# Kernel optimization log

Measured on AMD Instinct MI355X. Metric: run time of the kernel, lower is better.

Reference implementation:

```python
import jax, jax.numpy as jnp
import numpy as np


def _cheb_conv(x, row, col, norm, W, b, num_nodes):
    # PyG ChebConv with sym normalization and lambda_max=2:
    # L_hat = -D^{-1/2} A D^{-1/2} (off-diagonal), diagonal exactly 0.
    # Tx_0 = x; Tx_1 = L_hat x; Tx_k = 2 L_hat Tx_{k-1} - Tx_{k-2}
    K = W.shape[0]
    Tx0 = x
    out = Tx0 @ W[0]
    Tx1 = jax.ops.segment_sum(norm[:, None] * Tx0[col], row, num_segments=num_nodes)
    out = out + Tx1 @ W[1]
    for k in range(2, K):
        Tx2 = 2.0 * jax.ops.segment_sum(norm[:, None] * Tx1[col], row, num_segments=num_nodes) - Tx0
        out = out + Tx2 @ W[k]
        Tx0, Tx1 = Tx1, Tx2
    return out + b


def setup_inputs() -> dict:
    key = jax.random.key(0)
    ks = jax.random.split(key, 8)
    N, E, D, H, C, K = 100000, 1600000, 128, 64, 5, 3
    x = jax.random.normal(ks[0], (N, D), dtype=jnp.float32)
    edge_index = jax.random.randint(ks[1], (2, E), 0, N, dtype=jnp.int64)
    edge_weight = jax.random.uniform(ks[2], (E,), dtype=jnp.float32)
    s1 = 1.0 / np.sqrt(D)
    s3 = 1.0 / np.sqrt(H)
    W1 = jax.random.normal(ks[3], (K, D, H), dtype=jnp.float32) * s1
    W3 = jax.random.normal(ks[4], (K, H, H), dtype=jnp.float32) * s3
    W4 = jax.random.normal(ks[5], (K, H, C), dtype=jnp.float32) * s3
    return {
        "x": x, "edge_index": edge_index, "edge_weight": edge_weight,
        "W1": W1, "b1": jnp.zeros((H,), jnp.float32),
        "W3": W3, "b3": jnp.zeros((H,), jnp.float32),
        "W4": W4, "b4": jnp.zeros((C,), jnp.float32),
    }


def reference(x, edge_index, edge_weight, W1, b1, W3, b3, W4, b4):
    N = x.shape[0]
    row, col = edge_index[0], edge_index[1]
    # symmetric normalization of the scaled Laplacian (lambda_max = 2)
    deg = jax.ops.segment_sum(edge_weight, row, num_segments=N)
    dinv = jnp.where(deg > 0, jax.lax.rsqrt(jnp.where(deg > 0, deg, 1.0)), 0.0)
    norm = -dinv[row] * edge_weight * dinv[col]
    # dropout is a no-op in eval mode (training=False)
    h = jax.nn.relu(_cheb_conv(x, row, col, norm, W1, b1, N))
    h = jax.nn.relu(_cheb_conv(h, row, col, norm, W3, b3, N))
    h = _cheb_conv(h, row, col, norm, W4, b4, N)
    return jax.nn.log_softmax(h, axis=1)
```

## Files before the change

kernel.cpp:

```cpp
#include <hip/hip_runtime.h>
#include <cstdint>
#include <cstddef>

typedef unsigned short u16;
typedef __attribute__((ext_vector_type(8))) short bf16x8;
typedef __attribute__((ext_vector_type(4))) float f32x4;

#define PB 1024
#define MAXSB 256
#define SB 512
#define CAP 12288

__device__ __forceinline__ float bflo(unsigned u) { return __uint_as_float(u << 16); }
__device__ __forceinline__ float bfhi(unsigned u) { return __uint_as_float(u & 0xFFFF0000u); }
__device__ __forceinline__ u16 f2bf(float f) {
    unsigned u = __float_as_uint(f);
    u += 0x7FFFu + ((u >> 16) & 1u);
    return (u16)(u >> 16);
}
__device__ __forceinline__ unsigned pack2(float a, float b) {
    return (unsigned)f2bf(a) | ((unsigned)f2bf(b) << 16);
}


__global__ __launch_bounds__(256) void binA(const int* __restrict__ row, int* __restrict__ P,
                                            int E, int NB, int EB) {
    __shared__ int hist[MAXSB];
    int b = blockIdx.x;
    hist[threadIdx.x] = 0;
    __syncthreads();
    int e0 = b * EB, e1 = min(E, e0 + EB);
    for (int e = e0 + threadIdx.x; e < e1; e += 256)
        atomicAdd(&hist[row[e] >> 9], 1);
    __syncthreads();
    if (threadIdx.x < NB) P[(size_t)threadIdx.x * PB + b] = hist[threadIdx.x];
}

__global__ __launch_bounds__(256) void binB1(int* __restrict__ P, int* __restrict__ bintot) {
    __shared__ int sh[256];
    int* p = P + (size_t)blockIdx.x * PB;
    int tid = threadIdx.x;
    int base = tid * 4;
    int v[4];
#pragma unroll
    for (int j = 0; j < 4; ++j) v[j] = p[base + j];
    int s = v[0] + v[1] + v[2] + v[3];
    sh[tid] = s;
    __syncthreads();
    for (int off = 1; off < 256; off <<= 1) {
        int t = (tid >= off) ? sh[tid - off] : 0;
        __syncthreads();
        sh[tid] += t;
        __syncthreads();
    }
    int run = sh[tid] - s;
#pragma unroll
    for (int j = 0; j < 4; ++j) { p[base + j] = run; run += v[j]; }
    if (tid == 255) bintot[blockIdx.x] = sh[255];
}

__device__ __forceinline__ void bs_scan(int* bs, const int* bintot, int NB, int tid) {
    bs[tid] = (tid < NB) ? bintot[tid] : 0;
    __syncthreads();
    for (int off = 1; off < 256; off <<= 1) {
        int t = (tid >= off) ? bs[tid - off] : 0;
        __syncthreads();
        bs[tid] += t;
        __syncthreads();
    }
}

__global__ __launch_bounds__(256) void binC(const int* __restrict__ row, const int* __restrict__ col,
                                            const float* __restrict__ w, const int* __restrict__ P,
                                            const int* __restrict__ bintot, int2* __restrict__ rec,
                                            int E, int NB, int EB) {
    __shared__ int bs[MAXSB];
    __shared__ int cur[MAXSB];
    int b = blockIdx.x;
    int tid = threadIdx.x;
    bs_scan(bs, bintot, NB, tid);
    if (tid < NB) cur[tid] = (tid ? bs[tid - 1] : 0) + P[(size_t)tid * PB + b];
    __syncthreads();
    int e0 = b * EB, e1 = min(E, e0 + EB);
    for (int e = e0 + tid; e < e1; e += 256) {
        int r = row[e];
        int bin = r >> 9;
        int slot = atomicAdd(&cur[bin], 1);
        rec[slot] = make_int2(col[e] | ((r & 511) << 17), __float_as_int(w[e]));
    }
}

__global__ __launch_bounds__(256) void binD1(const int2* __restrict__ rec,
                                             const int* __restrict__ bintot,
                                             int* __restrict__ rowp, float* __restrict__ dinv,
                                             int N, int NB) {
    __shared__ int bs[MAXSB];
    __shared__ int cnt[SB];
    __shared__ float deg[SB];
    __shared__ int wsum[4];
    int bin = blockIdx.x;
    int tid = threadIdx.x;
    bs_scan(bs, bintot, NB, tid);
    int e0 = bin ? bs[bin - 1] : 0;
    int e1 = bs[bin];
    cnt[tid] = 0; cnt[tid + 256] = 0;
    deg[tid] = 0.f; deg[tid + 256] = 0.f;
    __syncthreads();
    for (int e = e0 + tid; e < e1; e += 256) {
        int2 v = rec[e];
        int rl = (v.x >> 17) & 511;
        atomicAdd(&cnt[rl], 1);
        atomicAdd(&deg[rl], __int_as_float(v.y));
    }
    __syncthreads();
    int a = cnt[2 * tid], b = cnt[2 * tid + 1];
    int p = a + b;
    int lane = tid & 63, wv = tid >> 6;
    int incl = p;
    for (int off = 1; off < 64; off <<= 1) {
        int t = __shfl_up(incl, off);
        if (lane >= off) incl += t;
    }
    if (lane == 63) wsum[wv] = incl;
    __syncthreads();
    if (tid == 0) {
        int s = 0;
#pragma unroll
        for (int i = 0; i < 4; ++i) { int t = wsum[i]; wsum[i] = s; s += t; }
    }
    __syncthreads();
    int excl = incl - p + wsum[wv];
    int base = bin * SB;
    int rows = min(SB, N - base);
    if (2 * tid < rows) {
        rowp[base + 2 * tid] = e0 + excl;
        float d = deg[2 * tid];
        dinv[base + 2 * tid] = d > 0.f ? rsqrtf(d) : 0.f;
    }
    if (2 * tid + 1 < rows) {
        rowp[base + 2 * tid + 1] = e0 + excl + a;
        float d = deg[2 * tid + 1];
        dinv[base + 2 * tid + 1] = d > 0.f ? rsqrtf(d) : 0.f;
    }
    if (bin == NB - 1 && tid == 0) rowp[N] = e1;
}

__global__ __launch_bounds__(256) void binD2(const int2* __restrict__ rec,
                                             const int* __restrict__ bintot,
                                             const int* __restrict__ rowp,
                                             const float* __restrict__ dinv,
                                             int2* __restrict__ meta, int N, int NB) {
    __shared__ int bs[MAXSB];
    __shared__ int cur[SB];
    __shared__ int perm[CAP];
    int bin = blockIdx.x;
    int tid = threadIdx.x;
    bs_scan(bs, bintot, NB, tid);
    int e0 = bin ? bs[bin - 1] : 0;
    int e1 = bs[bin];
    int base = bin * SB;
    int rows = min(SB, N - base);
    for (int i = tid; i < rows; i += 256) cur[i] = rowp[base + i];
    __syncthreads();
    for (int e = e0 + tid; e < e1; e += 256) {
        int2 v = rec[e];
        int rl = (v.x >> 17) & 511;
        int slot = atomicAdd(&cur[rl], 1);
        int so = slot - e0;
        if (so < CAP) {
            perm[so] = e - e0;
        } else {
            int c = v.x & 0x1FFFF;
            float ev = -dinv[base + rl] * __int_as_float(v.y) * dinv[c];
            meta[slot] = make_int2(c, __float_as_int(ev));
        }
    }
    __syncthreads();
    int lim = min(e1 - e0, CAP);
    for (int s = tid; s < lim; s += 256) {
        int2 v = rec[e0 + perm[s]];
        int rl = (v.x >> 17) & 511;
        int c = v.x & 0x1FFFF;
        float ev = -dinv[base + rl] * __int_as_float(v.y) * dinv[c];
        meta[e0 + s] = make_int2(c, __float_as_int(ev));
    }
}

__global__ void prep(const float* __restrict__ x, unsigned* __restrict__ xb, int n2,
                     const float* __restrict__ W1, const float* __restrict__ W3,
                     const float* __restrict__ W4, u16* __restrict__ Wpu,
                     u16* __restrict__ Wp3, u16* __restrict__ Wpp) {
    int gi = blockIdx.x * blockDim.x + threadIdx.x;
    if (gi < 3072) {
        int idx = gi;
        int lane = idx & 63;
        int nt = (idx >> 6) % 12;
        int kt = idx / 768;
        int krow = kt * 32 + (lane >> 4) * 8;
        int c = nt * 16 + (lane & 15);
        u16 tmp[8];
#pragma unroll
        for (int j = 0; j < 8; ++j) {
            int k = krow + j;
            float v;
            if (c < 64)       v = W1[(size_t)k * 64 + c] - W1[2 * 8192 + (size_t)k * 64 + c];
            else if (c < 128) v = W1[8192 + (size_t)k * 64 + (c - 64)];
            else              v = W1[2 * 8192 + (size_t)k * 64 + (c - 128)];
            tmp[j] = f2bf(v);
        }
        *reinterpret_cast<uint4*>(Wpu + (size_t)idx * 8) = *reinterpret_cast<const uint4*>(tmp);
    } else if (gi < 3072 + 1536) {
        int idx = gi - 3072;
        int lane = idx & 63;
        int nt = (idx >> 6) & 3;
        int kt = idx >> 8;
        int krow = kt * 32 + (lane >> 4) * 8;
        int c = nt * 16 + (lane & 15);
        u16 tmp[8];
#pragma unroll
        for (int j = 0; j < 8; ++j) tmp[j] = f2bf(W3[(size_t)(krow + j) * 64 + c]);
        *reinterpret_cast<uint4*>(Wp3 + (size_t)idx * 8) = *reinterpret_cast<const uint4*>(tmp);
    } else if (gi < 3072 + 1536 + 256) {
        int idx = gi - (3072 + 1536);
        int lane = idx & 63;
        int nt = (idx >> 6) & 1;
        int kt = idx >> 7;
        int krow = kt * 32 + (lane >> 4) * 8;
        int c = nt * 16 + (lane & 15);
        u16 tmp[8];
#pragma unroll
        for (int j = 0; j < 8; ++j) {
            int k = krow + j;
            float v = 0.f;
            if (c < 5)                  v = W4[(size_t)k * 5 + c] - W4[640 + (size_t)k * 5 + c];
            else if (c >= 8 && c < 13)  v = W4[320 + (size_t)k * 5 + (c - 8)];
            else if (c >= 16 && c < 21) v = W4[640 + (size_t)k * 5 + (c - 16)];
            tmp[j] = f2bf(v);
        }
        *reinterpret_cast<uint4*>(Wpp + (size_t)idx * 8) = *reinterpret_cast<const uint4*>(tmp);
    } else {
        int i = gi - 4864;
        if (i < n2) {
            float2 v = reinterpret_cast<const float2*>(x)[i];
            xb[i] = pack2(v.x, v.y);
        }
    }
}

template <int MODE>
__global__ __launch_bounds__(256) void spmm64(const int* __restrict__ rp,
                                              const int2* __restrict__ meta,
                                              const u16* __restrict__ x,
                                              const u16* __restrict__ z,
                                              const float* __restrict__ bias,
                                              u16* __restrict__ y, int n) {
    int r = blockIdx.x * 16 + (threadIdx.x >> 4);
    if (r >= n) return;
    int sub = (threadIdx.x >> 3) & 1;
    int f = (threadIdx.x & 7) * 8;
    int e0 = rp[r], e1 = rp[r + 1];
    float acc[8] = {0.f, 0.f, 0.f, 0.f, 0.f, 0.f, 0.f, 0.f};
    auto fma8 = [&](uint4 xv, float w) {
        acc[0] += w * bflo(xv.x); acc[1] += w * bfhi(xv.x);
        acc[2] += w * bflo(xv.y); acc[3] += w * bfhi(xv.y);
        acc[4] += w * bflo(xv.z); acc[5] += w * bfhi(xv.z);
        acc[6] += w * bflo(xv.w); acc[7] += w * bfhi(xv.w);
    };
    int e = e0 + sub;
    for (; e + 6 < e1; e += 8) {
        int2 m0 = meta[e], m1 = meta[e + 2], m2 = meta[e + 4], m3 = meta[e + 6];
        uint4 v0 = *reinterpret_cast<const uint4*>(x + (size_t)m0.x * 64 + f);
        uint4 v1 = *reinterpret_cast<const uint4*>(x + (size_t)m1.x * 64 + f);
        uint4 v2 = *reinterpret_cast<const uint4*>(x + (size_t)m2.x * 64 + f);
        uint4 v3 = *reinterpret_cast<const uint4*>(x + (size_t)m3.x * 64 + f);
        fma8(v0, __int_as_float(m0.y));
        fma8(v1, __int_as_float(m1.y));
        fma8(v2, __int_as_float(m2.y));
        fma8(v3, __int_as_float(m3.y));
    }
    for (; e < e1; e += 2) {
        int2 m = meta[e];
        uint4 xv = *reinterpret_cast<const uint4*>(x + (size_t)m.x * 64 + f);
        fma8(xv, __int_as_float(m.y));
    }
#pragma unroll
    for (int j = 0; j < 8; ++j) acc[j] += __shfl_xor(acc[j], 8);
    if (sub) return;
    if (MODE == 1 || MODE == 2) {
        uint4 zv = *reinterpret_cast<const uint4*>(z + (size_t)r * 64 + f);
        float zz[8] = {bflo(zv.x), bfhi(zv.x), bflo(zv.y), bfhi(zv.y),
                       bflo(zv.z), bfhi(zv.z), bflo(zv.w), bfhi(zv.w)};
#pragma unroll
        for (int j = 0; j < 8; ++j)
            acc[j] = (MODE == 1) ? 2.f * acc[j] + zz[j] : 2.f * acc[j] - zz[j];
    } else if (MODE == 3) {
        uint4 zv = *reinterpret_cast<const uint4*>(z + (size_t)r * 64 + f);
        float zz[8] = {bflo(zv.x), bfhi(zv.x), bflo(zv.y), bfhi(zv.y),
                       bflo(zv.z), bfhi(zv.z), bflo(zv.w), bfhi(zv.w)};
        float4 bl = *reinterpret_cast<const float4*>(bias + f);
        float4 bh = *reinterpret_cast<const float4*>(bias + f + 4);
        float bb[8] = {bl.x, bl.y, bl.z, bl.w, bh.x, bh.y, bh.z, bh.w};
#pragma unroll
        for (int j = 0; j < 8; ++j) acc[j] = fmaxf(acc[j] + zz[j] + bb[j], 0.f);
    }
    uint4 o;
    o.x = pack2(acc[0], acc[1]);
    o.y = pack2(acc[2], acc[3]);
    o.z = pack2(acc[4], acc[5]);
    o.w = pack2(acc[6], acc[7]);
    *reinterpret_cast<uint4*>(y + (size_t)r * 64 + f) = o;
}

__device__ __forceinline__ void spmm8_acc(const int* rp, const int2* meta, const u16* x,
                                          int r, int t, float* acc) {
    int e0 = rp[r], e1 = rp[r + 1];
    auto fma8 = [&](uint4 xv, float w) {
        acc[0] += w * bflo(xv.x); acc[1] += w * bfhi(xv.x);
        acc[2] += w * bflo(xv.y); acc[3] += w * bfhi(xv.y);
        acc[4] += w * bflo(xv.z); acc[5] += w * bfhi(xv.z);
        acc[6] += w * bflo(xv.w); acc[7] += w * bfhi(xv.w);
    };
    int e = e0 + t;
    for (; e + 4 < e1; e += 8) {
        int2 m0 = meta[e], m1 = meta[e + 4];
        uint4 v0 = *reinterpret_cast<const uint4*>(x + (size_t)m0.x * 8);
        uint4 v1 = *reinterpret_cast<const uint4*>(x + (size_t)m1.x * 8);
        fma8(v0, __int_as_float(m0.y));
        fma8(v1, __int_as_float(m1.y));
    }
    for (; e < e1; e += 4) {
        int2 m = meta[e];
        uint4 xv = *reinterpret_cast<const uint4*>(x + (size_t)m.x * 8);
        fma8(xv, __int_as_float(m.y));
    }
#pragma unroll
    for (int j = 0; j < 8; ++j) acc[j] += __shfl_xor(acc[j], 1);
#pragma unroll
    for (int j = 0; j < 8; ++j) acc[j] += __shfl_xor(acc[j], 2);
}

__global__ __launch_bounds__(256) void spmm8_p2(const int* __restrict__ rp,
                                                const int2* __restrict__ meta,
                                                const u16* __restrict__ x,
                                                const u16* __restrict__ z,
                                                u16* __restrict__ y, int n) {
    int r = blockIdx.x * 64 + (threadIdx.x >> 2);
    if (r >= n) return;
    int t = threadIdx.x & 3;
    float acc[8] = {0.f, 0.f, 0.f, 0.f, 0.f, 0.f, 0.f, 0.f};
    spmm8_acc(rp, meta, x, r, t, acc);
    if (t == 0) {
        uint4 zv = *reinterpret_cast<const uint4*>(z + (size_t)r * 8);
        float zz[8] = {bflo(zv.x), bfhi(zv.x), bflo(zv.y), bfhi(zv.y),
                       bflo(zv.z), bfhi(zv.z), bflo(zv.w), bfhi(zv.w)};
        uint4 o;
        o.x = pack2(2.f * acc[0] + zz[0], 2.f * acc[1] + zz[1]);
        o.y = pack2(2.f * acc[2] + zz[2], 2.f * acc[3] + zz[3]);
        o.z = pack2(2.f * acc[4] + zz[4], 2.f * acc[5] + zz[5]);
        o.w = pack2(2.f * acc[6] + zz[6], 2.f * acc[7] + zz[7]);
        *reinterpret_cast<uint4*>(y + (size_t)r * 8) = o;
    }
}

__global__ __launch_bounds__(256) void spmm8_lsm(const int* __restrict__ rp,
                                                 const int2* __restrict__ meta,
                                                 const u16* __restrict__ x,
                                                 const u16* __restrict__ z,
                                                 const float* __restrict__ bias,
                                                 float* __restrict__ out, int n) {
    int r = blockIdx.x * 64 + (threadIdx.x >> 2);
    if (r >= n) return;
    int t = threadIdx.x & 3;
    float acc[8] = {0.f, 0.f, 0.f, 0.f, 0.f, 0.f, 0.f, 0.f};
    spmm8_acc(rp, meta, x, r, t, acc);
    if (t == 0) {
        uint4 zv = *reinterpret_cast<const uint4*>(z + (size_t)r * 8);
        float zz[8] = {bflo(zv.x), bfhi(zv.x), bflo(zv.y), bfhi(zv.y),
                       bflo(zv.z), bfhi(zv.z), bflo(zv.w), bfhi(zv.w)};
        float val[5];
#pragma unroll
        for (int j = 0; j < 5; ++j) val[j] = acc[j] + zz[j] + bias[j];
        float mx = val[0];
#pragma unroll
        for (int j = 1; j < 5; ++j) mx = fmaxf(mx, val[j]);
        float s = 0.f;
#pragma unroll
        for (int j = 0; j < 5; ++j) s += expf(val[j] - mx);
        float l = logf(s);
#pragma unroll
        for (int j = 0; j < 5; ++j) out[(size_t)r * 5 + j] = val[j] - mx - l;
    }
}


__global__ __launch_bounds__(256) void gemm_u(const u16* __restrict__ A,
                                              const u16* __restrict__ Wp,
                                              u16* __restrict__ u0, u16* __restrict__ u1,
                                              u16* __restrict__ u2, int n) {
    int wave = threadIdx.x >> 6;
    int lane = threadIdx.x & 63;
    int r0 = blockIdx.x * 64 + wave * 16;
    int row = r0 + (lane & 15);
    int rowc = row < n ? row : n - 1;
    int kofs = (lane >> 4) * 8;
    f32x4 acc[12] = {};
    for (int kt = 0; kt < 4; ++kt) {
        bf16x8 a = *reinterpret_cast<const bf16x8*>(A + (size_t)rowc * 128 + kt * 32 + kofs);
        const u16* wb = Wp + (size_t)kt * 12 * 512 + (size_t)lane * 8;
#pragma unroll
        for (int nt = 0; nt < 12; ++nt) {
            bf16x8 b = *reinterpret_cast<const bf16x8*>(wb + nt * 512);
            acc[nt] = __builtin_amdgcn_mfma_f32_16x16x32_bf16(a, b, acc[nt], 0, 0, 0);
        }
    }
    int col = lane & 15;
    u16* U[3] = {u0, u1, u2};
#pragma unroll
    for (int nt = 0; nt < 12; ++nt) {
        u16* dst = U[nt >> 2];
        int cc = (nt & 3) * 16 + col;
#pragma unroll
        for (int i = 0; i < 4; ++i) {
            int rr = r0 + (lane >> 4) * 4 + i;
            if (rr < n) dst[(size_t)rr * 64 + cc] = f2bf(acc[nt][i]);
        }
    }
}

__global__ __launch_bounds__(256) void gemm3_mfma(const u16* __restrict__ A0,
                                                  const u16* __restrict__ A1,
                                                  const u16* __restrict__ A2,
                                                  const u16* __restrict__ Wp,
                                                  const float* __restrict__ bias,
                                                  u16* __restrict__ out, int n) {
    int wave = threadIdx.x >> 6;
    int lane = threadIdx.x & 63;
    int r0 = blockIdx.x * 64 + wave * 16;
    int row = r0 + (lane & 15);
    int rowc = row < n ? row : n - 1;
    int kofs = (lane >> 4) * 8;
    const u16* Ap[3] = {A0, A1, A2};
    f32x4 acc[4] = {};
    for (int kt = 0; kt < 6; ++kt) {
        const u16* Asrc = Ap[kt >> 1];
        int c0 = (kt & 1) * 32;
        bf16x8 a = *reinterpret_cast<const bf16x8*>(Asrc + (size_t)rowc * 64 + c0 + kofs);
        const u16* wb = Wp + (size_t)kt * 4 * 512 + (size_t)lane * 8;
#pragma unroll
        for (int nt = 0; nt < 4; ++nt) {
            bf16x8 b = *reinterpret_cast<const bf16x8*>(wb + nt * 512);
            acc[nt] = __builtin_amdgcn_mfma_f32_16x16x32_bf16(a, b, acc[nt], 0, 0, 0);
        }
    }
    int col = lane & 15;
#pragma unroll
    for (int nt = 0; nt < 4; ++nt) {
        float bb = bias[nt * 16 + col];
#pragma unroll
        for (int i = 0; i < 4; ++i) {
            int rr = r0 + (lane >> 4) * 4 + i;
            if (rr < n) {
                float v = fmaxf(acc[nt][i] + bb, 0.f);
                out[(size_t)rr * 64 + nt * 16 + col] = f2bf(v);
            }
        }
    }
}

__global__ __launch_bounds__(256) void gemm_proj(const u16* __restrict__ A,
                                                 const u16* __restrict__ Wp,
                                                 u16* __restrict__ p0, u16* __restrict__ p1,
                                                 u16* __restrict__ p2, int n) {
    int wave = threadIdx.x >> 6;
    int lane = threadIdx.x & 63;
    int r0 = blockIdx.x * 64 + wave * 16;
    int row = r0 + (lane & 15);
    int rowc = row < n ? row : n - 1;
    int kofs = (lane >> 4) * 8;
    f32x4 acc[2] = {};
    for (int kt = 0; kt < 2; ++kt) {
        bf16x8 a = *reinterpret_cast<const bf16x8*>(A + (size_t)rowc * 64 + kt * 32 + kofs);
        const u16* wb = Wp + (size_t)kt * 2 * 512 + (size_t)lane * 8;
#pragma unroll
        for (int nt = 0; nt < 2; ++nt) {
            bf16x8 b = *reinterpret_cast<const bf16x8*>(wb + nt * 512);
            acc[nt] = __builtin_amdgcn_mfma_f32_16x16x32_bf16(a, b, acc[nt], 0, 0, 0);
        }
    }
    int col = lane & 15;
    u16* P[3] = {p0, p1, p2};
#pragma unroll
    for (int nt = 0; nt < 2; ++nt) {
        int c = nt * 16 + col;
        if (c < 24) {
            u16* dst = P[c >> 3];
            int j = c & 7;
#pragma unroll
            for (int i = 0; i < 4; ++i) {
                int rr = r0 + (lane >> 4) * 4 + i;
                if (rr < n) dst[(size_t)rr * 8 + j] = f2bf(acc[nt][i]);
            }
        }
    }
}


static inline size_t alignup(size_t v) { return (v + 255) & ~(size_t)255; }

extern "C" void kernel_launch(void* const* d_in, const int* in_sizes, int n_in,
                              void* d_out, int out_size, void* d_ws, size_t ws_size,
                              hipStream_t stream) {
    const float* x  = (const float*)d_in[0];
    const int*   ei = (const int*)d_in[1];
    const float* ew = (const float*)d_in[2];
    const float* W1 = (const float*)d_in[3];
    const float* b1 = (const float*)d_in[4];
    const float* W3 = (const float*)d_in[5];
    const float* b3 = (const float*)d_in[6];
    const float* W4 = (const float*)d_in[7];
    const float* b4 = (const float*)d_in[8];
    float* out = (float*)d_out;

    const int D = 128, H = 64;
    const int N = in_sizes[0] / D;
    const int E = in_sizes[2];
    const int* row = ei;
    const int* col = ei + E;

    char* ws = (char*)d_ws;
    size_t off = 0;
    auto alloc = [&](size_t bytes) { size_t o = off; off += alignup(bytes); return o; };

    float* dinv   = (float*)(ws + alloc((size_t)N * 4));
    int*   rowp   = (int*)  (ws + alloc((size_t)(N + 1) * 4));
    int*   bintot = (int*)  (ws + alloc(MAXSB * 4));
    int*   P      = (int*)  (ws + alloc((size_t)MAXSB * PB * 4));
    int2*  meta   = (int2*) (ws + alloc((size_t)E * 8));
    int2*  rec    = (int2*) (ws + alloc((size_t)E * 8));
    u16*   xb     = (u16*)  (ws + alloc((size_t)N * D * 2));
    u16*   A      = (u16*)  (ws + alloc((size_t)N * H * 2));
    u16*   B      = (u16*)  (ws + alloc((size_t)N * H * 2));
    u16*   C      = (u16*)  (ws + alloc((size_t)N * H * 2));
    u16*   Dd     = (u16*)  (ws + alloc((size_t)N * H * 2));
    u16*   P0     = (u16*)  (ws + alloc((size_t)N * 8 * 2));
    u16*   P1     = (u16*)  (ws + alloc((size_t)N * 8 * 2));
    u16*   P2     = (u16*)  (ws + alloc((size_t)N * 8 * 2));
    u16*   P3     = (u16*)  (ws + alloc((size_t)N * 8 * 2));
    u16*   Wpu    = (u16*)  (ws + alloc((size_t)4 * 12 * 512 * 2));
    u16*   Wp3    = (u16*)  (ws + alloc((size_t)6 * 4 * 512 * 2));
    u16*   Wpp    = (u16*)  (ws + alloc((size_t)2 * 2 * 512 * 2));

    const int NB = (N + SB - 1) / SB;
    const int EB = (E + PB - 1) / PB;

    dim3 blk(256);

    binA<<<PB, blk, 0, stream>>>(row, P, E, NB, EB);
    binB1<<<NB, blk, 0, stream>>>(P, bintot);
    binC<<<PB, blk, 0, stream>>>(row, col, ew, P, bintot, rec, E, NB, EB);
    binD1<<<NB, blk, 0, stream>>>(rec, bintot, rowp, dinv, N, NB);
    binD2<<<NB, blk, 0, stream>>>(rec, bintot, rowp, dinv, meta, N, NB);

    int n2 = N * D / 2;
    prep<<<(n2 + 4864 + 255) / 256, blk, 0, stream>>>(x, (unsigned*)xb, n2, W1, W3, W4,
                                                      Wpu, Wp3, Wpp);

    int g64 = (N + 15) / 16;
    int gG  = (N + 63) / 64;
    int g8  = (N + 63) / 64;

    gemm_u<<<gG, blk, 0, stream>>>(xb, Wpu, A, B, C, N);
    spmm64<1><<<g64, blk, 0, stream>>>(rowp, meta, C, B, nullptr, Dd, N);
    spmm64<3><<<g64, blk, 0, stream>>>(rowp, meta, Dd, A, b1, B, N);

    spmm64<0><<<g64, blk, 0, stream>>>(rowp, meta, B, nullptr, nullptr, C, N);
    spmm64<2><<<g64, blk, 0, stream>>>(rowp, meta, C, B, nullptr, A, N);
    gemm3_mfma<<<gG, blk, 0, stream>>>(B, C, A, Wp3, b3, Dd, N);

    gemm_proj<<<gG, blk, 0, stream>>>(Dd, Wpp, P0, P1, P2, N);
    spmm8_p2<<<g8, blk, 0, stream>>>(rowp, meta, P2, P1, P3, N);
    spmm8_lsm<<<g8, blk, 0, stream>>>(rowp, meta, P3, P0, b4, out, N);
}
```

Before: 285.2 us.

## Fuse x bf16 conversion into gemm_u and projection GEMM into layer-2 GEMM

Drops the separate pass that converts x from fp32 to bf16; gemm_u now reads fp32 x directly and converts in registers. Fuses gemm_proj into gemm3 by staging the relu'd hidden tile in shared memory, so the intermediate 64-wide hidden matrix is never written to or read back from global memory. This removes the xb buffer traffic and one kernel launch, in exchange for a __syncthreads, LDS use and doubled fp32 read bandwidth in gemm_u.

```diff
diff --git a/kernel.cpp b/kernel.cpp
--- a/kernel.cpp
+++ b/kernel.cpp
@@ -186,8 +186,7 @@
     }
 }
 
-__global__ void prep(const float* __restrict__ x, unsigned* __restrict__ xb, int n2,
-                     const float* __restrict__ W1, const float* __restrict__ W3,
+__global__ void prep(const float* __restrict__ W1, const float* __restrict__ W3,
                      const float* __restrict__ W4, u16* __restrict__ Wpu,
                      u16* __restrict__ Wp3, u16* __restrict__ Wpp) {
     int gi = blockIdx.x * blockDim.x + threadIdx.x;
@@ -238,12 +237,6 @@
             tmp[j] = f2bf(v);
         }
         *reinterpret_cast<uint4*>(Wpp + (size_t)idx * 8) = *reinterpret_cast<const uint4*>(tmp);
-    } else {
-        int i = gi - 4864;
-        if (i < n2) {
-            float2 v = reinterpret_cast<const float2*>(x)[i];
-            xb[i] = pack2(v.x, v.y);
-        }
     }
 }
 
@@ -393,7 +386,7 @@
 }
 
 
-__global__ __launch_bounds__(256) void gemm_u(const u16* __restrict__ A,
+__global__ __launch_bounds__(256) void gemm_u(const float* __restrict__ X,
                                               const u16* __restrict__ Wp,
                                               u16* __restrict__ u0, u16* __restrict__ u1,
                                               u16* __restrict__ u2, int n) {
@@ -405,7 +398,12 @@
     int kofs = (lane >> 4) * 8;
     f32x4 acc[12] = {};
     for (int kt = 0; kt < 4; ++kt) {
-        bf16x8 a = *reinterpret_cast<const bf16x8*>(A + (size_t)rowc * 128 + kt * 32 + kofs);
+        const float* xs = X + (size_t)rowc * 128 + kt * 32 + kofs;
+        float4 xa = *reinterpret_cast<const float4*>(xs);
+        float4 xb4 = *reinterpret_cast<const float4*>(xs + 4);
+        u16 tmp[8] = {f2bf(xa.x), f2bf(xa.y), f2bf(xa.z), f2bf(xa.w),
+                      f2bf(xb4.x), f2bf(xb4.y), f2bf(xb4.z), f2bf(xb4.w)};
+        bf16x8 a = *reinterpret_cast<const bf16x8*>(tmp);
         const u16* wb = Wp + (size_t)kt * 12 * 512 + (size_t)lane * 8;
 #pragma unroll
         for (int nt = 0; nt < 12; ++nt) {
@@ -427,12 +425,15 @@
     }
 }
 
-__global__ __launch_bounds__(256) void gemm3_mfma(const u16* __restrict__ A0,
-                                                  const u16* __restrict__ A1,
-                                                  const u16* __restrict__ A2,
-                                                  const u16* __restrict__ Wp,
-                                                  const float* __restrict__ bias,
-                                                  u16* __restrict__ out, int n) {
+__global__ __launch_bounds__(256) void gemm3_fused(const u16* __restrict__ A0,
+                                                   const u16* __restrict__ A1,
+                                                   const u16* __restrict__ A2,
+                                                   const u16* __restrict__ Wp,
+                                                   const float* __restrict__ bias,
+                                                   const u16* __restrict__ Wpp,
+                                                   u16* __restrict__ p0, u16* __restrict__ p1,
+                                                   u16* __restrict__ p2, int n) {
+    __shared__ u16 hl[64][72];
     int wave = threadIdx.x >> 6;
     int lane = threadIdx.x & 63;
     int r0 = blockIdx.x * 64 + wave * 16;
@@ -458,36 +459,22 @@
         float bb = bias[nt * 16 + col];
 #pragma unroll
         for (int i = 0; i < 4; ++i) {
-            int rr = r0 + (lane >> 4) * 4 + i;
-            if (rr < n) {
-                float v = fmaxf(acc[nt][i] + bb, 0.f);
-                out[(size_t)rr * 64 + nt * 16 + col] = f2bf(v);
-            }
-        }
-    }
-}
-
-__global__ __launch_bounds__(256) void gemm_proj(const u16* __restrict__ A,
-                                                 const u16* __restrict__ Wp,
-                                                 u16* __restrict__ p0, u16* __restrict__ p1,
-                                                 u16* __restrict__ p2, int n) {
-    int wave = threadIdx.x >> 6;
-    int lane = threadIdx.x & 63;
-    int r0 = blockIdx.x * 64 + wave * 16;
-    int row = r0 + (lane & 15);
-    int rowc = row < n ? row : n - 1;
-    int kofs = (lane >> 4) * 8;
-    f32x4 acc[2] = {};
+            float v = fmaxf(acc[nt][i] + bb, 0.f);
+            hl[wave * 16 + (lane >> 4) * 4 + i][nt * 16 + col] = f2bf(v);
+        }
+    }
+    __syncthreads();
+    f32x4 acc2[2] = {};
+#pragma unroll
     for (int kt = 0; kt < 2; ++kt) {
-        bf16x8 a = *reinterpret_cast<const bf16x8*>(A + (size_t)rowc * 64 + kt * 32 + kofs);
-        const u16* wb = Wp + (size_t)kt * 2 * 512 + (size_t)lane * 8;
+        bf16x8 a = *reinterpret_cast<const bf16x8*>(&hl[wave * 16 + (lane & 15)][kt * 32 + kofs]);
+        const u16* wb = Wpp + (size_t)kt * 2 * 512 + (size_t)lane * 8;
 #pragma unroll
         for (int nt = 0; nt < 2; ++nt) {
             bf16x8 b = *reinterpret_cast<const bf16x8*>(wb + nt * 512);
-            acc[nt] = __builtin_amdgcn_mfma_f32_16x16x32_bf16(a, b, acc[nt], 0, 0, 0);
-        }
-    }
-    int col = lane & 15;
+            acc2[nt] = __builtin_amdgcn_mfma_f32_16x16x32_bf16(a, b, acc2[nt], 0, 0, 0);
+        }
+    }
     u16* P[3] = {p0, p1, p2};
 #pragma unroll
     for (int nt = 0; nt < 2; ++nt) {
@@ -498,7 +485,7 @@
 #pragma unroll
             for (int i = 0; i < 4; ++i) {
                 int rr = r0 + (lane >> 4) * 4 + i;
-                if (rr < n) dst[(size_t)rr * 8 + j] = f2bf(acc[nt][i]);
+                if (rr < n) dst[(size_t)rr * 8 + j] = f2bf(acc2[nt][i]);
             }
         }
     }
@@ -537,7 +524,6 @@
     int*   P      = (int*)  (ws + alloc((size_t)MAXSB * PB * 4));
     int2*  meta   = (int2*) (ws + alloc((size_t)E * 8));
     int2*  rec    = (int2*) (ws + alloc((size_t)E * 8));
-    u16*   xb     = (u16*)  (ws + alloc((size_t)N * D * 2));
     u16*   A      = (u16*)  (ws + alloc((size_t)N * H * 2));
     u16*   B      = (u16*)  (ws + alloc((size_t)N * H * 2));
     u16*   C      = (u16*)  (ws + alloc((size_t)N * H * 2));
@@ -561,23 +547,20 @@
     binD1<<<NB, blk, 0, stream>>>(rec, bintot, rowp, dinv, N, NB);
     binD2<<<NB, blk, 0, stream>>>(rec, bintot, rowp, dinv, meta, N, NB);
 
-    int n2 = N * D / 2;
-    prep<<<(n2 + 4864 + 255) / 256, blk, 0, stream>>>(x, (unsigned*)xb, n2, W1, W3, W4,
-                                                      Wpu, Wp3, Wpp);
+    prep<<<(4864 + 255) / 256, blk, 0, stream>>>(W1, W3, W4, Wpu, Wp3, Wpp);
 
     int g64 = (N + 15) / 16;
     int gG  = (N + 63) / 64;
     int g8  = (N + 63) / 64;
 
-    gemm_u<<<gG, blk, 0, stream>>>(xb, Wpu, A, B, C, N);
+    gemm_u<<<gG, blk, 0, stream>>>(x, Wpu, A, B, C, N);
     spmm64<1><<<g64, blk, 0, stream>>>(rowp, meta, C, B, nullptr, Dd, N);
     spmm64<3><<<g64, blk, 0, stream>>>(rowp, meta, Dd, A, b1, B, N);
 
     spmm64<0><<<g64, blk, 0, stream>>>(rowp, meta, B, nullptr, nullptr, C, N);
     spmm64<2><<<g64, blk, 0, stream>>>(rowp, meta, C, B, nullptr, A, N);
-    gemm3_mfma<<<gG, blk, 0, stream>>>(B, C, A, Wp3, b3, Dd, N);
-
-    gemm_proj<<<gG, blk, 0, stream>>>(Dd, Wpp, P0, P1, P2, N);
+    gemm3_fused<<<gG, blk, 0, stream>>>(B, C, A, Wp3, b3, Wpp, P0, P1, P2, N);
+
     spmm8_p2<<<g8, blk, 0, stream>>>(rowp, meta, P2, P1, P3, N);
     spmm8_lsm<<<g8, blk, 0, stream>>>(rowp, meta, P3, P0, b4, out, N);
 }
```

Result: faster. 266.8 us (median of 2 runs) (-6.5%).
